# Optimization experiments

Hardware: AMD Instinct MI355X
Metric: run time of the kernel (lower is better)

## Reference

```python
import jax, jax.numpy as jnp
import numpy as np

M, I, J = 524288, 16, 16


def setup_inputs() -> dict:
    key = jax.random.key(0)
    k1, k2, k3, k4 = jax.random.split(key, 4)
    h = jax.random.normal(k1, (2, 1, 1, I, J), dtype=jnp.float32)
    gi = jax.random.normal(k2, (2, M, 1, I), dtype=jnp.float32)
    gj = jax.random.normal(k3, (2, 1, M, J), dtype=jnp.float32)
    theta = jax.random.uniform(k4, (2, M), dtype=jnp.float32) * (2.0 * np.pi)
    return {"h": h, "gi": gi, "gj": gj, "theta": theta}


def reference(h, gi, gj, theta):
    # Theta = diag(cos(theta[0])) + 1j * diag(sin(theta[1])) -- diagonal, so the
    # per-(i,j) bilinear form gj_j @ Theta @ gi_i is an O(M) contraction.
    tre = jnp.cos(theta[0])  # [M]
    tim = jnp.sin(theta[1])  # [M]
    a, b = gj[0, 0], gj[1, 0]            # [M, J] real/imag of gj
    e, f = gi[0, :, 0, :], gi[1, :, 0, :]  # [M, I] real/imag of gi
    # u = Theta_diag * gj (complex elementwise along M)
    u_re = a * tre[:, None] - b * tim[:, None]  # [M, J]
    u_im = a * tim[:, None] + b * tre[:, None]  # [M, J]
    # out[i,j] = sum_m gi[m,i] * theta[m] * gj[m,j] (complex)
    out_re = jnp.einsum('mi,mj->ij', e, u_re) - jnp.einsum('mi,mj->ij', f, u_im)
    out_im = jnp.einsum('mi,mj->ij', e, u_im) + jnp.einsum('mi,mj->ij', f, u_re)
    # htilde = h + reflected path, then squeeze the singleton dims -> [2, I, J]
    return h[:, 0, 0] + jnp.stack([out_re, out_im], axis=0)
```

## Files before the change

### kernel.cpp

```cpp
#include <hip/hip_runtime.h>


constexpr int MDIM    = 524288;
constexpr int THREADS = 256;
constexpr int BLOCKS  = 512;
constexpr int M_PER_B = MDIM / BLOCKS;
constexpr int M_PER_W = M_PER_B / 4;
constexpr int CHUNK   = 16;
constexpr int NCH     = M_PER_W / CHUNK;
constexpr int DEPTH   = 3;

constexpr int E_OFF = 0, F_OFF = 256, A_OFF = 512, B_OFF = 768;
constexpr int T0_OFF = 1024, T1_OFF = 1040;
constexpr int BUF_F  = 1056;
constexpr int WAVE_F = DEPTH * BUF_F;
constexpr int SMEM_F = 4 * WAVE_F;
static_assert(SMEM_F * sizeof(float) <= 65536, "LDS must stay under 64 KiB");

typedef float f32x2 __attribute__((ext_vector_type(2)));

#define AS1 __attribute__((address_space(1)))
#define AS3 __attribute__((address_space(3)))

__device__ __forceinline__ void cp16(const float* g, float* l) {
    __builtin_amdgcn_global_load_lds((const AS1 void*)g, (AS3 void*)l, 16, 0, 0);
}
__device__ __forceinline__ void cp4(const float* g, float* l) {
    __builtin_amdgcn_global_load_lds((const AS1 void*)g, (AS3 void*)l, 4, 0, 0);
}

__device__ __forceinline__ void stage(
    const float* e_g, const float* f_g, const float* a_g, const float* b_g,
    const float* t0_g, const float* t1_g, float* buf, int p, int lane)
{
    const size_t mo = (size_t)p * (CHUNK * 16);
    cp16(e_g + mo, buf + E_OFF);
    cp16(f_g + mo, buf + F_OFF);
    cp16(a_g + mo, buf + A_OFF);
    cp16(b_g + mo, buf + B_OFF);
    if (lane < 16) {
        cp4(t0_g + (size_t)p * CHUNK, buf + T0_OFF);
        cp4(t1_g + (size_t)p * CHUNK, buf + T1_OFF);
    }
}

__device__ __forceinline__ void compute_chunk(
    const float* buf, int slot, int i0, int j0,
    f32x2 (&are)[4][2], f32x2 (&aim)[4][2])
{
#pragma unroll
    for (int k = 0; k < 4; ++k) {
        const int ml = slot + 4 * k;
        const float4 e4 = *(const float4*)(buf + E_OFF + ml * 16 + i0);
        const float4 f4 = *(const float4*)(buf + F_OFF + ml * 16 + i0);
        const float4 a4 = *(const float4*)(buf + A_OFF + ml * 16 + j0);
        const float4 b4 = *(const float4*)(buf + B_OFF + ml * 16 + j0);
        const float c = __cosf(buf[T0_OFF + ml]);
        const float s = __sinf(buf[T1_OFF + ml]);
        const f32x2 cc = {c, c}, ss = {s, s};
        const f32x2 a01 = {a4.x, a4.y}, a23 = {a4.z, a4.w};
        const f32x2 b01 = {b4.x, b4.y}, b23 = {b4.z, b4.w};
        f32x2 ure[2], uim[2];
        ure[0] = __builtin_elementwise_fma(-b01, ss, a01 * cc);
        ure[1] = __builtin_elementwise_fma(-b23, ss, a23 * cc);
        uim[0] = __builtin_elementwise_fma( b01, cc, a01 * ss);
        uim[1] = __builtin_elementwise_fma( b23, cc, a23 * ss);
        const float ev[4] = {e4.x, e4.y, e4.z, e4.w};
        const float fv[4] = {f4.x, f4.y, f4.z, f4.w};
#pragma unroll
        for (int i = 0; i < 4; ++i) {
            const f32x2 ee = {ev[i], ev[i]};
            const f32x2 ff = {fv[i], fv[i]};
#pragma unroll
            for (int jp = 0; jp < 2; ++jp) {
                are[i][jp] = __builtin_elementwise_fma( ee, ure[jp], are[i][jp]);
                are[i][jp] = __builtin_elementwise_fma(-ff, uim[jp], are[i][jp]);
                aim[i][jp] = __builtin_elementwise_fma( ee, uim[jp], aim[i][jp]);
                aim[i][jp] = __builtin_elementwise_fma( ff, ure[jp], aim[i][jp]);
            }
        }
    }
}

template <bool USE_ATOMIC>
__device__ __forceinline__ void theta_body(
    const float* __restrict__ gi, const float* __restrict__ gj,
    const float* __restrict__ theta, float* __restrict__ dst)
{
    __shared__ float smem[SMEM_F];
    const int t    = threadIdx.x;
    const int wave = t >> 6;
    const int lane = t & 63;
    const int slot = (lane >> 4) & 3;
    const int tile = lane & 15;
    const int i0   = (tile >> 2) << 2;
    const int j0   = (tile & 3) << 2;
    const int m_w0 = blockIdx.x * M_PER_B + wave * M_PER_W;
    float* wbase   = smem + wave * WAVE_F;

    const float* e_g  = gi + (size_t)m_w0 * 16 + lane * 4;
    const float* f_g  = e_g + (size_t)MDIM * 16;
    const float* a_g  = gj + (size_t)m_w0 * 16 + lane * 4;
    const float* b_g  = a_g + (size_t)MDIM * 16;
    const float* t0_g = theta + m_w0 + lane;
    const float* t1_g = t0_g + MDIM;

    f32x2 are[4][2], aim[4][2];
#pragma unroll
    for (int i = 0; i < 4; ++i)
#pragma unroll
        for (int jp = 0; jp < 2; ++jp) { are[i][jp] = {0.f, 0.f}; aim[i][jp] = {0.f, 0.f}; }

    stage(e_g, f_g, a_g, b_g, t0_g, t1_g, wbase + 0 * BUF_F, 0, lane);
    stage(e_g, f_g, a_g, b_g, t0_g, t1_g, wbase + 1 * BUF_F, 1, lane);

    int sb = 2, cb = 0;
    for (int c = 0; c < NCH - 2; ++c) {
        stage(e_g, f_g, a_g, b_g, t0_g, t1_g, wbase + sb * BUF_F, c + 2, lane);
        sb = (sb == DEPTH - 1) ? 0 : sb + 1;
        asm volatile("s_waitcnt vmcnt(12)" ::: "memory");
        compute_chunk(wbase + cb * BUF_F, slot, i0, j0, are, aim);
        cb = (cb == DEPTH - 1) ? 0 : cb + 1;
    }
    asm volatile("s_waitcnt vmcnt(6)" ::: "memory");
    compute_chunk(wbase + cb * BUF_F, slot, i0, j0, are, aim);
    cb = (cb == DEPTH - 1) ? 0 : cb + 1;
    asm volatile("s_waitcnt vmcnt(0)" ::: "memory");
    compute_chunk(wbase + cb * BUF_F, slot, i0, j0, are, aim);

    float sre[4][4], sim[4][4];
#pragma unroll
    for (int i = 0; i < 4; ++i)
#pragma unroll
        for (int jp = 0; jp < 2; ++jp) {
            sre[i][jp * 2]     = are[i][jp].x;  sre[i][jp * 2 + 1] = are[i][jp].y;
            sim[i][jp * 2]     = aim[i][jp].x;  sim[i][jp * 2 + 1] = aim[i][jp].y;
        }

#pragma unroll
    for (int i = 0; i < 4; ++i)
#pragma unroll
        for (int j = 0; j < 4; ++j) {
            sre[i][j] += __shfl_xor(sre[i][j], 16);
            sre[i][j] += __shfl_xor(sre[i][j], 32);
            sim[i][j] += __shfl_xor(sim[i][j], 16);
            sim[i][j] += __shfl_xor(sim[i][j], 32);
        }

    __syncthreads();
    float (*red)[16][33] = (float (*)[16][33])smem;
    if (lane < 16) {
#pragma unroll
        for (int i = 0; i < 4; ++i)
#pragma unroll
            for (int j = 0; j < 4; ++j) {
                red[wave][lane][i * 4 + j]      = sre[i][j];
                red[wave][lane][16 + i * 4 + j] = sim[i][j];
            }
    }
    __syncthreads();

#pragma unroll
    for (int k = 0; k < 2; ++k) {
        const int idx = t * 2 + k;
        const int tl  = idx >> 5;
        const int v   = idx & 31;
        const float sum = red[0][tl][v] + red[1][tl][v] + red[2][tl][v] + red[3][tl][v];
        const int ii  = ((tl >> 2) << 2) + ((v & 15) >> 2);
        const int jj  = ((tl & 3) << 2) + (v & 3);
        const int off = ((v & 16) ? 256 : 0) + ii * 16 + jj;
        if (USE_ATOMIC) atomicAdd(dst + off, sum);
        else            dst[blockIdx.x * 512 + off] = sum;
    }
}

__global__ __launch_bounds__(THREADS) void theta_main_ws(
    const float* __restrict__ gi, const float* __restrict__ gj,
    const float* __restrict__ theta, float* __restrict__ partial)
{
    theta_body<false>(gi, gj, theta, partial);
}

__global__ __launch_bounds__(THREADS) void theta_main_atomic(
    const float* __restrict__ gi, const float* __restrict__ gj,
    const float* __restrict__ theta, float* __restrict__ out)
{
    theta_body<true>(gi, gj, theta, out);
}

__global__ __launch_bounds__(256) void theta_reduce(
    const float* __restrict__ h, const float* __restrict__ partial,
    float* __restrict__ out)
{
    const int w    = (blockIdx.x * 256 + threadIdx.x) >> 6;
    const int lane = threadIdx.x & 63;
    float s = 0.f;
#pragma unroll 4
    for (int j = 0; j < BLOCKS / 64; ++j)
        s += partial[(size_t)(j * 64 + lane) * 512 + w];
#pragma unroll
    for (int d = 1; d < 64; d <<= 1) s += __shfl_xor(s, d);
    if (lane == 0) out[w] = h[w] + s;
}

__global__ void theta_init(const float* __restrict__ h, float* __restrict__ out) {
    int k = blockIdx.x * blockDim.x + threadIdx.x;
    if (k < 512) out[k] = h[k];
}

extern "C" void kernel_launch(void* const* d_in, const int* in_sizes, int n_in,
                              void* d_out, int out_size, void* d_ws, size_t ws_size,
                              hipStream_t stream) {
    const float* h     = (const float*)d_in[0];
    const float* gi    = (const float*)d_in[1];
    const float* gj    = (const float*)d_in[2];
    const float* theta = (const float*)d_in[3];
    float* out = (float*)d_out;

    const size_t need = (size_t)BLOCKS * 512 * sizeof(float);
    if (ws_size >= need) {
        float* partial = (float*)d_ws;
        theta_main_ws<<<BLOCKS, THREADS, 0, stream>>>(gi, gj, theta, partial);
        theta_reduce<<<128, 256, 0, stream>>>(h, partial, out);
    } else {
        theta_init<<<2, 256, 0, stream>>>(h, out);
        theta_main_atomic<<<BLOCKS, THREADS, 0, stream>>>(gi, gj, theta, out);
    }
}
```

Before: 159.0 us.

## Share block-wide LDS pipeline with per-wave stream loading and barriers

Replaces the per-wave private triple-buffered pipeline with one block-wide triple buffer of 64-row chunks. Each wave now streams one input array (e, f, a or b, with theta on two waves) into shared LDS, and all waves compute on the combined chunk after a block barrier. The aim is larger, more contiguous per-wave loads with fewer address streams per wave. The cost is two __syncthreads per chunk, which couple the waves and can expose load latency.

```diff
diff --git a/kernel.cpp b/kernel.cpp
--- a/kernel.cpp
+++ b/kernel.cpp
@@ -5,17 +5,17 @@
 constexpr int THREADS = 256;
 constexpr int BLOCKS  = 512;
 constexpr int M_PER_B = MDIM / BLOCKS;
-constexpr int M_PER_W = M_PER_B / 4;
-constexpr int CHUNK   = 16;
-constexpr int NCH     = M_PER_W / CHUNK;
+constexpr int CHUNK   = 64;
+constexpr int NCH     = M_PER_B / CHUNK;
 constexpr int DEPTH   = 3;
-
-constexpr int E_OFF = 0, F_OFF = 256, A_OFF = 512, B_OFF = 768;
-constexpr int T0_OFF = 1024, T1_OFF = 1040;
-constexpr int BUF_F  = 1056;
-constexpr int WAVE_F = DEPTH * BUF_F;
-constexpr int SMEM_F = 4 * WAVE_F;
-static_assert(SMEM_F * sizeof(float) <= 65536, "LDS must stay under 64 KiB");
+static_assert(NCH * BLOCKS * CHUNK == MDIM, "exact tiling");
+static_assert(NCH >= DEPTH, "pipeline fill");
+
+constexpr int E_OFF = 0, F_OFF = 1024, A_OFF = 2048, B_OFF = 3072;
+constexpr int T0_OFF = 4096, T1_OFF = 4160;
+constexpr int BUF_F  = 4224;
+constexpr int SMEM_F = DEPTH * BUF_F;
+static_assert(SMEM_F * sizeof(float) <= 65536, "LDS < 64 KiB");
 
 typedef float f32x2 __attribute__((ext_vector_type(2)));
 
@@ -29,35 +29,35 @@
     __builtin_amdgcn_global_load_lds((const AS1 void*)g, (AS3 void*)l, 4, 0, 0);
 }
 
+#define WAITV(n) asm volatile("s_waitcnt vmcnt(" #n ")" ::: "memory")
+
 __device__ __forceinline__ void stage(
-    const float* e_g, const float* f_g, const float* a_g, const float* b_g,
-    const float* t0_g, const float* t1_g, float* buf, int p, int lane)
-{
-    const size_t mo = (size_t)p * (CHUNK * 16);
-    cp16(e_g + mo, buf + E_OFF);
-    cp16(f_g + mo, buf + F_OFF);
-    cp16(a_g + mo, buf + A_OFF);
-    cp16(b_g + mo, buf + B_OFF);
-    if (lane < 16) {
-        cp4(t0_g + (size_t)p * CHUNK, buf + T0_OFF);
-        cp4(t1_g + (size_t)p * CHUNK, buf + T1_OFF);
-    }
+    float* buf, const float* src, const float* tsrc,
+    int soff, int toff, int p, int lane)
+{
+    const float* s = src + (size_t)p * (CHUNK * 16) + lane * 4;
+    float* d = buf + soff;
+#pragma unroll
+    for (int q = 0; q < 4; ++q)
+        cp16(s + q * 256, d + q * 256);
+    if (tsrc)
+        cp4(tsrc + (size_t)p * CHUNK + lane, buf + toff);
 }
 
 __device__ __forceinline__ void compute_chunk(
-    const float* buf, int slot, int i0, int j0,
+    const float* buf, int wave, int slot, int i0, int j0,
     f32x2 (&are)[4][2], f32x2 (&aim)[4][2])
 {
 #pragma unroll
     for (int k = 0; k < 4; ++k) {
-        const int ml = slot + 4 * k;
+        const int ml = wave * 4 + slot + 16 * k;
         const float4 e4 = *(const float4*)(buf + E_OFF + ml * 16 + i0);
         const float4 f4 = *(const float4*)(buf + F_OFF + ml * 16 + i0);
         const float4 a4 = *(const float4*)(buf + A_OFF + ml * 16 + j0);
         const float4 b4 = *(const float4*)(buf + B_OFF + ml * 16 + j0);
-        const float c = __cosf(buf[T0_OFF + ml]);
-        const float s = __sinf(buf[T1_OFF + ml]);
-        const f32x2 cc = {c, c}, ss = {s, s};
+        const float cv = __cosf(buf[T0_OFF + ml]);
+        const float sv = __sinf(buf[T1_OFF + ml]);
+        const f32x2 cc = {cv, cv}, ss = {sv, sv};
         const f32x2 a01 = {a4.x, a4.y}, a23 = {a4.z, a4.w};
         const f32x2 b01 = {b4.x, b4.y}, b23 = {b4.z, b4.w};
         f32x2 ure[2], uim[2];
@@ -95,15 +95,14 @@
     const int tile = lane & 15;
     const int i0   = (tile >> 2) << 2;
     const int j0   = (tile & 3) << 2;
-    const int m_w0 = blockIdx.x * M_PER_B + wave * M_PER_W;
-    float* wbase   = smem + wave * WAVE_F;
-
-    const float* e_g  = gi + (size_t)m_w0 * 16 + lane * 4;
-    const float* f_g  = e_g + (size_t)MDIM * 16;
-    const float* a_g  = gj + (size_t)m_w0 * 16 + lane * 4;
-    const float* b_g  = a_g + (size_t)MDIM * 16;
-    const float* t0_g = theta + m_w0 + lane;
-    const float* t1_g = t0_g + MDIM;
+    const size_t mB = (size_t)blockIdx.x * M_PER_B;
+
+    const float* src;  const float* tsrc = nullptr;
+    int soff, toff = 0;
+    if      (wave == 0) { src = gi + mB * 16;                     soff = E_OFF; tsrc = theta + mB;        toff = T0_OFF; }
+    else if (wave == 1) { src = gi + (size_t)MDIM * 16 + mB * 16; soff = F_OFF; tsrc = theta + MDIM + mB; toff = T1_OFF; }
+    else if (wave == 2) { src = gj + mB * 16;                     soff = A_OFF; }
+    else                { src = gj + (size_t)MDIM * 16 + mB * 16; soff = B_OFF; }
 
     f32x2 are[4][2], aim[4][2];
 #pragma unroll
@@ -111,22 +110,22 @@
 #pragma unroll
         for (int jp = 0; jp < 2; ++jp) { are[i][jp] = {0.f, 0.f}; aim[i][jp] = {0.f, 0.f}; }
 
-    stage(e_g, f_g, a_g, b_g, t0_g, t1_g, wbase + 0 * BUF_F, 0, lane);
-    stage(e_g, f_g, a_g, b_g, t0_g, t1_g, wbase + 1 * BUF_F, 1, lane);
-
-    int sb = 2, cb = 0;
-    for (int c = 0; c < NCH - 2; ++c) {
-        stage(e_g, f_g, a_g, b_g, t0_g, t1_g, wbase + sb * BUF_F, c + 2, lane);
-        sb = (sb == DEPTH - 1) ? 0 : sb + 1;
-        asm volatile("s_waitcnt vmcnt(12)" ::: "memory");
-        compute_chunk(wbase + cb * BUF_F, slot, i0, j0, are, aim);
+    stage(smem + 0 * BUF_F, src, tsrc, soff, toff, 0, lane);
+    stage(smem + 1 * BUF_F, src, tsrc, soff, toff, 1, lane);
+    stage(smem + 2 * BUF_F, src, tsrc, soff, toff, 2, lane);
+
+    int cb = 0;
+    for (int c = 0; c < NCH; ++c) {
+        if (c <= NCH - 3) { if (wave < 2) WAITV(10); else WAITV(8); }
+        else if (c == NCH - 2) { if (wave < 2) WAITV(5); else WAITV(4); }
+        else { WAITV(0); }
+        __syncthreads();
+        compute_chunk(smem + cb * BUF_F, wave, slot, i0, j0, are, aim);
+        __syncthreads();
+        if (c + 3 < NCH)
+            stage(smem + cb * BUF_F, src, tsrc, soff, toff, c + 3, lane);
         cb = (cb == DEPTH - 1) ? 0 : cb + 1;
     }
-    asm volatile("s_waitcnt vmcnt(6)" ::: "memory");
-    compute_chunk(wbase + cb * BUF_F, slot, i0, j0, are, aim);
-    cb = (cb == DEPTH - 1) ? 0 : cb + 1;
-    asm volatile("s_waitcnt vmcnt(0)" ::: "memory");
-    compute_chunk(wbase + cb * BUF_F, slot, i0, j0, are, aim);
 
     float sre[4][4], sim[4][4];
 #pragma unroll
```

New measurement: 162.8 us. 1.02x slower.
